# Kernel tuning notes

Measured on AMD Instinct MI355X. Metric: run time of the kernel, lower is better.

## Reference

```python
import jax, jax.numpy as jnp
import numpy as np

N_NODES = 500_000
DIM_IN = 128
DIM_OUT = 128
N_DISTRICTS = 1024


def setup_inputs() -> dict:
    key = jax.random.key(0)
    k_x, k_z, k_w1, k_w2 = jax.random.split(key, 4)
    x = jax.random.normal(k_x, (N_NODES, DIM_IN), dtype=jnp.float32)
    zone_lst = jax.random.randint(k_z, (N_NODES,), 0, N_DISTRICTS, dtype=jnp.int64)
    # MLP params: Linear(dim_in, 2*dim_in), Linear(2*dim_in, dim_out)
    w1 = jax.random.normal(k_w1, (DIM_IN, 2 * DIM_IN), dtype=jnp.float32) * (1.0 / np.sqrt(DIM_IN))
    b1 = jnp.zeros((2 * DIM_IN,), dtype=jnp.float32)
    w2 = jax.random.normal(k_w2, (2 * DIM_IN, DIM_OUT), dtype=jnp.float32) * (1.0 / np.sqrt(2 * DIM_IN))
    b2 = jnp.zeros((DIM_OUT,), dtype=jnp.float32)
    return {"x": x, "zone_lst": zone_lst, "w1": w1, "b1": b1, "w2": w2, "b2": b2}


def reference(x, zone_lst, w1, b1, w2, b2):
    # Per-district sum of node features: one fused segment reduction
    # (replaces the python loop over districts in the original).
    head = jax.ops.segment_sum(x, zone_lst, num_segments=N_DISTRICTS)  # [D, dim_in]
    # MLP: ReLU -> Linear -> ReLU -> Linear
    h = jnp.maximum(head, 0.0)
    h = jnp.maximum(h @ w1 + b1, 0.0)
    return h @ w2 + b2
```

## Files before the change

kernel.cpp:

```cpp
#include <hip/hip_runtime.h>

#define DIM_IN 128
#define DIM_HID 256
#define DIM_OUT 128
#define N_DIST 1024
#define NB 256


__device__ __forceinline__ int detect_is64(const int* __restrict__ zone_raw,
                                           int t, int* s_flag) {
    if (t < 64) {
        bool hi_zero = (zone_raw[2 * t + 1] == 0);
        unsigned long long m = __ballot(hi_zero);
        if (t == 0) *s_flag = (m == ~0ull) ? 1 : 0;
    }
    __syncthreads();
    return *s_flag;
}

__global__ __launch_bounds__(256)
void hist_kernel(const int* __restrict__ zone, int n,
                 int* __restrict__ blockHist) {
    __shared__ int lhist[N_DIST];
    __shared__ int s_is64;
    const int t = threadIdx.x;
    const int b = blockIdx.x;
    for (int i = t; i < N_DIST; i += 256) lhist[i] = 0;
    const int is64 = detect_is64(zone, t, &s_is64);

    const int chunk = (n + NB - 1) / NB;
    const int start = b * chunk;
    const int end = min(n, start + chunk);
    const long long* zone64 = (const long long*)zone;
    for (int i = start + t; i < end; i += 256) {
        int z = is64 ? (int)zone64[i] : zone[i];
        atomicAdd(&lhist[z], 1);
    }
    __syncthreads();
    for (int i = t; i < N_DIST; i += 256) blockHist[b * N_DIST + i] = lhist[i];
}

__global__ __launch_bounds__(256)
void scanA_kernel(int* __restrict__ blockHist, int* __restrict__ counts) {
    const int t = threadIdx.x;
    const int lane = t & 63;
    const int w = t >> 6;
    const int d = blockIdx.x * 4 + w;

    int v0 = blockHist[(4 * lane + 0) * N_DIST + d];
    int v1 = blockHist[(4 * lane + 1) * N_DIST + d];
    int v2 = blockHist[(4 * lane + 2) * N_DIST + d];
    int v3 = blockHist[(4 * lane + 3) * N_DIST + d];
    const int tsum = v0 + v1 + v2 + v3;

    int s = tsum;
#pragma unroll
    for (int off = 1; off < 64; off <<= 1) {
        int u = __shfl_up(s, off);
        if (lane >= off) s += u;
    }
    const int total = __shfl(s, 63);
    int excl = s - tsum;

    blockHist[(4 * lane + 0) * N_DIST + d] = excl; excl += v0;
    blockHist[(4 * lane + 1) * N_DIST + d] = excl; excl += v1;
    blockHist[(4 * lane + 2) * N_DIST + d] = excl; excl += v2;
    blockHist[(4 * lane + 3) * N_DIST + d] = excl;

    if (lane == 0) counts[d] = total;
}

__global__ __launch_bounds__(256)
void scatter_kernel(const int* __restrict__ zone, int n,
                    const int* __restrict__ blockStart,
                    const int* __restrict__ counts,
                    int* __restrict__ offsets,
                    int* __restrict__ sorted) {
    __shared__ int off[N_DIST];
    __shared__ int lcur[N_DIST];
    __shared__ int wsum[4];
    __shared__ int s_is64;
    const int t = threadIdx.x;
    const int b = blockIdx.x;
    const int lane = t & 63;
    const int w = t >> 6;

    int4 c4 = ((const int4*)counts)[t];
    const int tsum = c4.x + c4.y + c4.z + c4.w;
    int s = tsum;
#pragma unroll
    for (int o = 1; o < 64; o <<= 1) {
        int u = __shfl_up(s, o);
        if (lane >= o) s += u;
    }
    if (lane == 63) wsum[w] = s;
    __syncthreads();
    int wbase = 0;
#pragma unroll
    for (int ww = 0; ww < 3; ww++) wbase += (ww < w) ? wsum[ww] : 0;
    int excl = wbase + s - tsum;
    off[4 * t + 0] = excl;
    off[4 * t + 1] = excl + c4.x;
    off[4 * t + 2] = excl + c4.x + c4.y;
    off[4 * t + 3] = excl + c4.x + c4.y + c4.z;
    __syncthreads();

    for (int i = t; i < N_DIST; i += 256)
        lcur[i] = off[i] + blockStart[b * N_DIST + i];
    if (b == 0)
        for (int i = t; i < N_DIST; i += 256) offsets[i] = off[i];

    const int is64 = detect_is64(zone, t, &s_is64);

    const int chunk = (n + NB - 1) / NB;
    const int start = b * chunk;
    const int end = min(n, start + chunk);
    const long long* zone64 = (const long long*)zone;
    for (int i = start + t; i < end; i += 256) {
        int z = is64 ? (int)zone64[i] : zone[i];
        int pos = atomicAdd(&lcur[z], 1);
        sorted[pos] = i;
    }
}

#define NG 16
__global__ __launch_bounds__(512)
void district_kernel(const float* __restrict__ x, const int* __restrict__ sorted,
                     const int* __restrict__ offsets, const int* __restrict__ counts,
                     const float* __restrict__ w1, const float* __restrict__ b1,
                     const float* __restrict__ w2, const float* __restrict__ b2,
                     float* __restrict__ out) {
    const int d = blockIdx.x;
    const int start = offsets[d];
    const int cnt = counts[d];
    const int t = threadIdx.x;
    const int q = t & 31;
    const int g = t >> 5;

    __shared__ int sidx[1024];

    const float* xq = x + (size_t)q * 4;
    float4 a0 = make_float4(0.f, 0.f, 0.f, 0.f);
    float4 a1 = a0, a2 = a0, a3 = a0;

    for (int base = 0; base < cnt; base += 1024) {
        const int m = min(cnt - base, 1024);
        for (int i = t; i < m; i += 512) sidx[i] = sorted[start + base + i];
        __syncthreads();

        int n = g;
        for (; n + 3 * NG < m; n += 4 * NG) {
            int i0 = sidx[n];
            int i1 = sidx[n + NG];
            int i2 = sidx[n + 2 * NG];
            int i3 = sidx[n + 3 * NG];
            float4 v0 = *(const float4*)(xq + (size_t)i0 * DIM_IN);
            float4 v1 = *(const float4*)(xq + (size_t)i1 * DIM_IN);
            float4 v2 = *(const float4*)(xq + (size_t)i2 * DIM_IN);
            float4 v3 = *(const float4*)(xq + (size_t)i3 * DIM_IN);
            a0.x += v0.x; a0.y += v0.y; a0.z += v0.z; a0.w += v0.w;
            a1.x += v1.x; a1.y += v1.y; a1.z += v1.z; a1.w += v1.w;
            a2.x += v2.x; a2.y += v2.y; a2.z += v2.z; a2.w += v2.w;
            a3.x += v3.x; a3.y += v3.y; a3.z += v3.z; a3.w += v3.w;
        }
        for (; n < m; n += NG) {
            int i0 = sidx[n];
            float4 v0 = *(const float4*)(xq + (size_t)i0 * DIM_IN);
            a0.x += v0.x; a0.y += v0.y; a0.z += v0.z; a0.w += v0.w;
        }
        __syncthreads();
    }

    a0.x += a1.x + a2.x + a3.x;
    a0.y += a1.y + a2.y + a3.y;
    a0.z += a1.z + a2.z + a3.z;
    a0.w += a1.w + a2.w + a3.w;

    __shared__ float part[NG][DIM_IN];
    part[g][q * 4 + 0] = a0.x;
    part[g][q * 4 + 1] = a0.y;
    part[g][q * 4 + 2] = a0.z;
    part[g][q * 4 + 3] = a0.w;
    __syncthreads();

    __shared__ float hrelu[DIM_IN];
    if (t < DIM_IN) {
        float s = 0.f;
#pragma unroll
        for (int gg = 0; gg < NG; gg++) s += part[gg][t];
        hrelu[t] = fmaxf(s, 0.f);
    }
    __syncthreads();

    {
        const int c = t & 255;
        const int h = t >> 8;
        float s1 = 0.f;
        const int k0 = h * 64;
#pragma unroll 8
        for (int k = k0; k < k0 + 64; k++) {
            s1 = fmaf(hrelu[k], w1[k * DIM_HID + c], s1);
        }
        __shared__ float p1[2][DIM_HID];
        p1[h][c] = s1;
        __syncthreads();
        __shared__ float h1s[DIM_HID];
        if (t < DIM_HID) h1s[t] = fmaxf(b1[t] + p1[0][t] + p1[1][t], 0.f);
        __syncthreads();

        const int c2 = t & 127;
        const int hh = t >> 7;
        float s2 = 0.f;
        const int j0 = hh * 64;
#pragma unroll 8
        for (int j = j0; j < j0 + 64; j++) {
            s2 = fmaf(h1s[j], w2[j * DIM_OUT + c2], s2);
        }
        __shared__ float p2[4][DIM_OUT];
        p2[hh][c2] = s2;
        __syncthreads();
        if (t < DIM_OUT)
            out[d * DIM_OUT + t] =
                b2[t] + p2[0][t] + p2[1][t] + p2[2][t] + p2[3][t];
    }
}

extern "C" void kernel_launch(void* const* d_in, const int* in_sizes, int n_in,
                              void* d_out, int out_size, void* d_ws, size_t ws_size,
                              hipStream_t stream) {
    const float* x    = (const float*)d_in[0];
    const int*   zone = (const int*)d_in[1];
    const float* w1   = (const float*)d_in[2];
    const float* b1   = (const float*)d_in[3];
    const float* w2   = (const float*)d_in[4];
    const float* b2   = (const float*)d_in[5];
    float* out = (float*)d_out;
    const int n = in_sizes[0] / DIM_IN;

    char* ws = (char*)d_ws;
    int* counts    = (int*)(ws);
    int* offsets   = (int*)(ws + 4096);
    int* blockHist = (int*)(ws + 65536);
    int* sorted    = (int*)(ws + (2u << 20));

    hist_kernel<<<NB, 256, 0, stream>>>(zone, n, blockHist);
    scanA_kernel<<<N_DIST / 4, 256, 0, stream>>>(blockHist, counts);
    scatter_kernel<<<NB, 256, 0, stream>>>(zone, n, blockHist, counts,
                                           offsets, sorted);
    district_kernel<<<N_DIST, 512, 0, stream>>>(x, sorted, offsets, counts,
                                                w1, b1, w2, b2, out);
}
```

Baseline: 382.6 us.

## Fuse histogram, scan and scatter into one cooperative kernel with grid syncs

Merges the three counting-sort kernels into one cooperative launch that separates the phases with grid-wide syncs instead of kernel boundaries. Each block also keeps its chunk of zone ids in shared memory as 16-bit values, so the scatter phase does not read zone from global memory a second time. This removes two launch gaps and one pass over the index array, at the cost of cooperative-launch overhead and grid-barrier latency. The sort phase is small next to the gather-heavy district kernel, so the total effect is limited.

```diff
diff --git a/kernel.cpp b/kernel.cpp
--- a/kernel.cpp
+++ b/kernel.cpp
@@ -1,10 +1,14 @@
 #include <hip/hip_runtime.h>
+#include <hip/hip_cooperative_groups.h>
+
+namespace cg = cooperative_groups;
 
 #define DIM_IN 128
 #define DIM_HID 256
 #define DIM_OUT 128
 #define N_DIST 1024
 #define NB 256
+#define CHUNK_MAX 2048
 
 
 __device__ __forceinline__ int detect_is64(const int* __restrict__ zone_raw,
@@ -19,107 +23,104 @@
 }
 
 __global__ __launch_bounds__(256)
-void hist_kernel(const int* __restrict__ zone, int n,
-                 int* __restrict__ blockHist) {
+void sort_kernel(const int* __restrict__ zone, int n,
+                 int* __restrict__ blockHist,
+                 int* __restrict__ counts,
+                 int* __restrict__ offsets,
+                 int* __restrict__ sorted) {
+    cg::grid_group grid = cg::this_grid();
     __shared__ int lhist[N_DIST];
-    __shared__ int s_is64;
-    const int t = threadIdx.x;
-    const int b = blockIdx.x;
-    for (int i = t; i < N_DIST; i += 256) lhist[i] = 0;
-    const int is64 = detect_is64(zone, t, &s_is64);
-
-    const int chunk = (n + NB - 1) / NB;
-    const int start = b * chunk;
-    const int end = min(n, start + chunk);
-    const long long* zone64 = (const long long*)zone;
-    for (int i = start + t; i < end; i += 256) {
-        int z = is64 ? (int)zone64[i] : zone[i];
-        atomicAdd(&lhist[z], 1);
-    }
-    __syncthreads();
-    for (int i = t; i < N_DIST; i += 256) blockHist[b * N_DIST + i] = lhist[i];
-}
-
-__global__ __launch_bounds__(256)
-void scanA_kernel(int* __restrict__ blockHist, int* __restrict__ counts) {
-    const int t = threadIdx.x;
-    const int lane = t & 63;
-    const int w = t >> 6;
-    const int d = blockIdx.x * 4 + w;
-
-    int v0 = blockHist[(4 * lane + 0) * N_DIST + d];
-    int v1 = blockHist[(4 * lane + 1) * N_DIST + d];
-    int v2 = blockHist[(4 * lane + 2) * N_DIST + d];
-    int v3 = blockHist[(4 * lane + 3) * N_DIST + d];
-    const int tsum = v0 + v1 + v2 + v3;
-
-    int s = tsum;
-#pragma unroll
-    for (int off = 1; off < 64; off <<= 1) {
-        int u = __shfl_up(s, off);
-        if (lane >= off) s += u;
-    }
-    const int total = __shfl(s, 63);
-    int excl = s - tsum;
-
-    blockHist[(4 * lane + 0) * N_DIST + d] = excl; excl += v0;
-    blockHist[(4 * lane + 1) * N_DIST + d] = excl; excl += v1;
-    blockHist[(4 * lane + 2) * N_DIST + d] = excl; excl += v2;
-    blockHist[(4 * lane + 3) * N_DIST + d] = excl;
-
-    if (lane == 0) counts[d] = total;
-}
-
-__global__ __launch_bounds__(256)
-void scatter_kernel(const int* __restrict__ zone, int n,
-                    const int* __restrict__ blockStart,
-                    const int* __restrict__ counts,
-                    int* __restrict__ offsets,
-                    int* __restrict__ sorted) {
-    __shared__ int off[N_DIST];
     __shared__ int lcur[N_DIST];
+    __shared__ unsigned short zc[CHUNK_MAX];
     __shared__ int wsum[4];
     __shared__ int s_is64;
+
     const int t = threadIdx.x;
     const int b = blockIdx.x;
     const int lane = t & 63;
     const int w = t >> 6;
 
-    int4 c4 = ((const int4*)counts)[t];
-    const int tsum = c4.x + c4.y + c4.z + c4.w;
-    int s = tsum;
-#pragma unroll
-    for (int o = 1; o < 64; o <<= 1) {
-        int u = __shfl_up(s, o);
-        if (lane >= o) s += u;
-    }
-    if (lane == 63) wsum[w] = s;
-    __syncthreads();
-    int wbase = 0;
-#pragma unroll
-    for (int ww = 0; ww < 3; ww++) wbase += (ww < w) ? wsum[ww] : 0;
-    int excl = wbase + s - tsum;
-    off[4 * t + 0] = excl;
-    off[4 * t + 1] = excl + c4.x;
-    off[4 * t + 2] = excl + c4.x + c4.y;
-    off[4 * t + 3] = excl + c4.x + c4.y + c4.z;
-    __syncthreads();
-
-    for (int i = t; i < N_DIST; i += 256)
-        lcur[i] = off[i] + blockStart[b * N_DIST + i];
-    if (b == 0)
-        for (int i = t; i < N_DIST; i += 256) offsets[i] = off[i];
-
+    for (int i = t; i < N_DIST; i += 256) lhist[i] = 0;
     const int is64 = detect_is64(zone, t, &s_is64);
 
     const int chunk = (n + NB - 1) / NB;
     const int start = b * chunk;
     const int end = min(n, start + chunk);
+    const bool cache_ok = (chunk <= CHUNK_MAX);
     const long long* zone64 = (const long long*)zone;
+
     for (int i = start + t; i < end; i += 256) {
         int z = is64 ? (int)zone64[i] : zone[i];
-        int pos = atomicAdd(&lcur[z], 1);
-        sorted[pos] = i;
+        if (cache_ok) zc[i - start] = (unsigned short)z;
+        atomicAdd(&lhist[z], 1);
+    }
+    __syncthreads();
+    for (int i = t; i < N_DIST; i += 256) blockHist[b * N_DIST + i] = lhist[i];
+
+    __threadfence();
+    grid.sync();
+
+    {
+        const int d = b * 4 + w;
+        int v0 = blockHist[(4 * lane + 0) * N_DIST + d];
+        int v1 = blockHist[(4 * lane + 1) * N_DIST + d];
+        int v2 = blockHist[(4 * lane + 2) * N_DIST + d];
+        int v3 = blockHist[(4 * lane + 3) * N_DIST + d];
+        const int tsum = v0 + v1 + v2 + v3;
+
+        int s = tsum;
+#pragma unroll
+        for (int off = 1; off < 64; off <<= 1) {
+            int u = __shfl_up(s, off);
+            if (lane >= off) s += u;
+        }
+        const int total = __shfl(s, 63);
+        int excl = s - tsum;
+
+        blockHist[(4 * lane + 0) * N_DIST + d] = excl; excl += v0;
+        blockHist[(4 * lane + 1) * N_DIST + d] = excl; excl += v1;
+        blockHist[(4 * lane + 2) * N_DIST + d] = excl; excl += v2;
+        blockHist[(4 * lane + 3) * N_DIST + d] = excl;
+
+        if (lane == 0) counts[d] = total;
+    }
+
+    __threadfence();
+    grid.sync();
+
+    {
+        int4 c4 = ((const int4*)counts)[t];
+        const int tsum = c4.x + c4.y + c4.z + c4.w;
+        int s = tsum;
+#pragma unroll
+        for (int o = 1; o < 64; o <<= 1) {
+            int u = __shfl_up(s, o);
+            if (lane >= o) s += u;
+        }
+        if (lane == 63) wsum[w] = s;
+        __syncthreads();
+        int wbase = 0;
+#pragma unroll
+        for (int ww = 0; ww < 3; ww++) wbase += (ww < w) ? wsum[ww] : 0;
+        int excl = wbase + s - tsum;
+        lhist[4 * t + 0] = excl;
+        lhist[4 * t + 1] = excl + c4.x;
+        lhist[4 * t + 2] = excl + c4.x + c4.y;
+        lhist[4 * t + 3] = excl + c4.x + c4.y + c4.z;
+        __syncthreads();
+
+        for (int i = t; i < N_DIST; i += 256)
+            lcur[i] = lhist[i] + blockHist[b * N_DIST + i];
+        if (b == 0)
+            for (int i = t; i < N_DIST; i += 256) offsets[i] = lhist[i];
+        __syncthreads();
+
+        for (int i = start + t; i < end; i += 256) {
+            int z = cache_ok ? (int)zc[i - start]
+                             : (is64 ? (int)zone64[i] : zone[i]);
+            int pos = atomicAdd(&lcur[z], 1);
+            sorted[pos] = i;
+        }
     }
 }
 
@@ -235,7 +236,7 @@
     const float* w2   = (const float*)d_in[4];
     const float* b2   = (const float*)d_in[5];
     float* out = (float*)d_out;
-    const int n = in_sizes[0] / DIM_IN;
+    int n = in_sizes[0] / DIM_IN;
 
     char* ws = (char*)d_ws;
     int* counts    = (int*)(ws);
@@ -243,10 +244,10 @@
     int* blockHist = (int*)(ws + 65536);
     int* sorted    = (int*)(ws + (2u << 20));
 
-    hist_kernel<<<NB, 256, 0, stream>>>(zone, n, blockHist);
-    scanA_kernel<<<N_DIST / 4, 256, 0, stream>>>(blockHist, counts);
-    scatter_kernel<<<NB, 256, 0, stream>>>(zone, n, blockHist, counts,
-                                           offsets, sorted);
+    void* args[] = { (void*)&zone, (void*)&n, (void*)&blockHist,
+                     (void*)&counts, (void*)&offsets, (void*)&sorted };
+    hipLaunchCooperativeKernel((const void*)sort_kernel, dim3(NB), dim3(256),
+                               args, 0, stream);
     district_kernel<<<N_DIST, 512, 0, stream>>>(x, sorted, offsets, counts,
                                                 w1, b1, w2, b2, out);
 }
```

Measured after the change: 505.7 us. 32.2% more time.
